# Performance work log

Measured on AMD Instinct MI355X. Metric: run time of the kernel, lower is better.

The kernel has to match this reference:

```python
import jax, jax.numpy as jnp
import numpy as np

N, E, D, H = 50000, 400000, 128, 4
NEG_SLOPE = 0.2
LN_EPS = 1e-5


def setup_inputs() -> dict:
    key = jax.random.key(0)
    ks = jax.random.split(key, 16)
    s = 1.0 / np.sqrt(D)
    inp = {
        'x': jax.random.normal(ks[0], (N, D), jnp.float32),
        'edge_index': jax.random.randint(ks[1], (2, E), 0, N, jnp.int32),
        # GATv2Conv params: lin_l/lin_r: Linear(D, H*D), att: [H, D], bias: [D] (concat=False)
        'Wl': jax.random.normal(ks[2], (H * D, D), jnp.float32) * s,
        'bl': jnp.zeros((H * D,), jnp.float32),
        'Wr': jax.random.normal(ks[3], (H * D, D), jnp.float32) * s,
        'br': jnp.zeros((H * D,), jnp.float32),
        'att': jax.random.normal(ks[4], (H, D), jnp.float32) * s,
        'bias': jnp.zeros((D,), jnp.float32),
        # LayerNorm 1
        'g1': jnp.ones((D,), jnp.float32), 'be1': jnp.zeros((D,), jnp.float32),
        # FFN: Linear(D, 2D) -> GELU -> Linear(2D, D)
        'W1': jax.random.normal(ks[5], (2 * D, D), jnp.float32) * s,
        'b1': jnp.zeros((2 * D,), jnp.float32),
        'W2': jax.random.normal(ks[6], (D, 2 * D), jnp.float32) * (1.0 / np.sqrt(2 * D)),
        'b2': jnp.zeros((D,), jnp.float32),
        # LayerNorm 2
        'g2': jnp.ones((D,), jnp.float32), 'be2': jnp.zeros((D,), jnp.float32),
    }
    return inp


def _layernorm(x, g, b):
    mu = jnp.mean(x, -1, keepdims=True)
    var = jnp.mean(jnp.square(x - mu), -1, keepdims=True)
    return (x - mu) * jax.lax.rsqrt(var + LN_EPS) * g + b


def _gatv2(x, edge_index, Wl, bl, Wr, br, att, bias):
    # Self-loops (PyG default add_self_loops=True)
    loop = jnp.arange(N, dtype=edge_index.dtype)
    src = jnp.concatenate([edge_index[0], loop])  # [E+N]
    dst = jnp.concatenate([edge_index[1], loop])
    xl = (x @ Wl.T + bl).reshape(N, H, D)  # source transform
    xr = (x @ Wr.T + br).reshape(N, H, D)  # target transform
    m = xl[src] + xr[dst]                  # [E+N, H, D]
    e = jnp.einsum('ehd,hd->eh', jax.nn.leaky_relu(m, NEG_SLOPE), att)
    # segment softmax over destination nodes
    emax = jax.ops.segment_max(e, dst, num_segments=N)
    ee = jnp.exp(e - emax[dst])
    denom = jax.ops.segment_sum(ee, dst, num_segments=N)
    alpha = ee / (denom[dst] + 1e-16)      # [E+N, H]  (dropout=0.1 skipped: eval mode)
    out = jax.ops.segment_sum(xl[src] * alpha[:, :, None], dst, num_segments=N)
    return out.mean(axis=1) + bias         # concat=False -> head mean


def reference(x, edge_index, Wl, bl, Wr, br, att, bias, g1, be1, W1, b1, W2, b2, g2, be2):
    h = _gatv2(x, edge_index, Wl, bl, Wr, br, att, bias)
    x = _layernorm(x + h, g1, be1)
    h = jax.nn.gelu(x @ W1.T + b1, approximate=False) @ W2.T + b2
    x = _layernorm(x + h, g2, be2)
    return x
```

## Files before the change

### kernel.cpp

```cpp
#include <hip/hip_runtime.h>
#include <cstdint>
#include <cstddef>

#define N_NODES 50000
#define N_EDGES 400000
#define EN_TOT  (N_EDGES + N_NODES)
#define NC_SCAN ((N_NODES + 511) / 512)
#define NEG_SLOPE 0.2f
#define LN_EPS 1e-5f

typedef short bf16x8 __attribute__((ext_vector_type(8)));
typedef float f32x4  __attribute__((ext_vector_type(4)));

__device__ __forceinline__ ushort f2bf(float f) {
    union { float f; uint32_t u; } c; c.f = f;
    uint32_t u = c.u + 0x7FFFu + ((c.u >> 16) & 1u);
    return (ushort)(u >> 16);
}
__device__ __forceinline__ uint32_t pk2(float a, float b) {
    return (uint32_t)f2bf(a) | ((uint32_t)f2bf(b) << 16);
}
__device__ __forceinline__ float bf_lo(uint32_t u) {
    union { uint32_t u; float f; } c; c.u = u << 16; return c.f;
}
__device__ __forceinline__ float bf_hi(uint32_t u) {
    union { uint32_t u; float f; } c; c.u = u & 0xFFFF0000u; return c.f;
}
__device__ __forceinline__ float bfu(const ushort* p) {
    union { uint32_t u; float f; } c; c.u = ((uint32_t)*p) << 16; return c.f;
}

__global__ __launch_bounds__(256) void prep(
    const float* __restrict__ Wl, const float* __restrict__ Wr,
    const float* __restrict__ W1, const float* __restrict__ W2,
    const float* __restrict__ att, ushort* __restrict__ wb,
    int* __restrict__ counts2 , int* __restrict__ state )
{
    int i = blockIdx.x * 256 + threadIdx.x;
    const float* src; int off;
    if (i < 65536)       { src = Wl;  off = i; }
    else if (i < 131072) { src = Wr;  off = i - 65536; }
    else if (i < 163840) { src = W1;  off = i - 131072; }
    else if (i < 196608) { src = W2;  off = i - 163840; }
    else                 { src = att; off = i - 196608; }
    wb[i] = f2bf(src[off]);
    if (i < 100000) counts2[i] = 0;
    if (i < 256)    state[i] = 0;
}

__global__ __launch_bounds__(256) void gemm_lr(
    const float* __restrict__ x, const ushort* __restrict__ wcat,
    const float* __restrict__ bl, const float* __restrict__ br,
    ushort* __restrict__ xlb, ushort* __restrict__ xrb)
{
    __shared__ ushort As[128 * 128];
    __shared__ ushort Bs[128 * 128];
    const int tid  = threadIdx.x;
    const int rb   = blockIdx.x * 128;
    const int wave = tid >> 6, lane = tid & 63;
    const int wm   = (wave >> 1) * 64, wn = (wave & 1) * 64;
    const int lr   = lane & 15, lq = lane >> 4;

    #pragma unroll
    for (int i = 0; i < 8; ++i) {
        int chunk = tid + i * 256;
        int rr = chunk >> 4, cc = chunk & 15;
        int gr = rb + rr;
        float4 v0 = make_float4(0.f,0.f,0.f,0.f), v1 = v0;
        if (gr < N_NODES) {
            v0 = *(const float4*)(x + (size_t)gr * 128 + cc * 8);
            v1 = *(const float4*)(x + (size_t)gr * 128 + cc * 8 + 4);
        }
        uint4 h = make_uint4(pk2(v0.x,v0.y), pk2(v0.z,v0.w),
                             pk2(v1.x,v1.y), pk2(v1.z,v1.w));
        *(uint4*)(As + rr * 128 + ((cc ^ (rr & 15)) * 8)) = h;
    }

    for (int cbk = 0; cbk < 8; ++cbk) {
        __syncthreads();
        #pragma unroll
        for (int i = 0; i < 8; ++i) {
            int chunk = tid + i * 256;
            int rr = chunk >> 4, cc = chunk & 15;
            uint4 vb = *(const uint4*)(wcat + (size_t)(cbk * 128 + rr) * 128 + cc * 8);
            *(uint4*)(Bs + rr * 128 + ((cc ^ (rr & 15)) * 8)) = vb;
        }
        __syncthreads();

        f32x4 zero = {0.f,0.f,0.f,0.f};
        f32x4 acc[4][4];
        #pragma unroll
        for (int i = 0; i < 4; ++i)
            #pragma unroll
            for (int j = 0; j < 4; ++j) acc[i][j] = zero;

        #pragma unroll
        for (int q = 0; q < 4; ++q) {
            int csw = ((q * 4 + lq) ^ lr) * 8;
            bf16x8 bfr[4], af[4];
            #pragma unroll
            for (int i = 0; i < 4; ++i) {
                bfr[i] = *(const bf16x8*)(Bs + (wm + i * 16 + lr) * 128 + csw);
                af[i]  = *(const bf16x8*)(As + (wn + i * 16 + lr) * 128 + csw);
            }
            #pragma unroll
            for (int i = 0; i < 4; ++i)
                #pragma unroll
                for (int j = 0; j < 4; ++j)
                    acc[i][j] = __builtin_amdgcn_mfma_f32_16x16x32_bf16(
                        bfr[i], af[j], acc[i][j], 0, 0, 0);
        }

        const float* bias = (cbk < 4) ? bl : br;
        ushort* outp = (cbk < 4) ? xlb : xrb;
        const int cloc = (cbk & 3) * 128;
        #pragma unroll
        for (int i = 0; i < 4; ++i) {
            int wc = wm + i * 16 + lq * 4;
            float4 bv = *(const float4*)(bias + cloc + wc);
            #pragma unroll
            for (int j = 0; j < 4; ++j) {
                int node = rb + wn + j * 16 + lr;
                if (node < N_NODES) {
                    ushort4 o;
                    o.x = f2bf(acc[i][j][0] + bv.x);
                    o.y = f2bf(acc[i][j][1] + bv.y);
                    o.z = f2bf(acc[i][j][2] + bv.z);
                    o.w = f2bf(acc[i][j][3] + bv.w);
                    *(ushort4*)(outp + (size_t)node * 512 + cloc + wc) = o;
                }
            }
        }
    }
}

__global__ __launch_bounds__(256) void count_deg(const int* __restrict__ dst,
                                                 int* __restrict__ counts)
{
    int i = blockIdx.x * 256 + threadIdx.x;
    if (i >= EN_TOT) return;
    int d = (i < N_EDGES) ? dst[i] : (i - N_EDGES);
    atomicAdd(counts + d, 1);
}

__global__ __launch_bounds__(64) void scan_lb(const int* __restrict__ counts,
                                              int* __restrict__ offs,
                                              unsigned long long* __restrict__ state)
{
    const int b = blockIdx.x, lane = threadIdx.x;
    const int base = b * 512 + lane * 8;
    int cnt[8];
    int s = 0;
    #pragma unroll
    for (int k = 0; k < 8; ++k) {
        int idx = base + k;
        cnt[k] = (idx < N_NODES) ? counts[idx] : 0;
        s += cnt[k];
    }
    int inc = s;
    #pragma unroll
    for (int d = 1; d < 64; d <<= 1) {
        int t = __shfl_up(inc, d, 64);
        if (lane >= d) inc += t;
    }
    const int total = __shfl(inc, 63, 64);

    if (lane == 0) {
        unsigned long long pub = ((unsigned long long)(b == 0 ? 2u : 1u) << 32)
                               | (unsigned)total;
        atomicExch(&state[b], pub);
    }

    int prefix = 0;
    if (b > 0) {
        int p0 = b - 1;
        while (true) {
            int p = p0 - lane;
            int flag, val;
            if (p >= 0) {
                unsigned long long v;
                do { v = atomicAdd(&state[p], 0ULL); flag = (int)(v >> 32); }
                while (flag == 0);
                val = (int)(unsigned)v;
            } else { flag = 2; val = 0; }
            unsigned long long mask = __ballot(flag == 2);
            int L = mask ? (__ffsll(mask) - 1) : 64;
            int take = (lane <= L) ? val : 0;
            #pragma unroll
            for (int m = 32; m; m >>= 1) take += __shfl_xor(take, m, 64);
            prefix += take;
            if (L < 64) break;
            p0 -= 64;
        }
        if (lane == 0)
            atomicExch(&state[b], (2ULL << 32) | (unsigned)(prefix + total));
    }

    int run = prefix + inc - s;
    #pragma unroll
    for (int k = 0; k < 8; ++k) {
        int idx = base + k;
        if (idx < N_NODES) { offs[idx] = run; run += cnt[k]; }
    }
    if (b == NC_SCAN - 1 && lane == 63) offs[N_NODES] = prefix + inc;
}

__global__ __launch_bounds__(256) void scatter_edges(
    const int* __restrict__ src, const int* __restrict__ dst,
    const int* __restrict__ offs, int* __restrict__ cursor,
    int* __restrict__ srcList)
{
    int i = blockIdx.x * 256 + threadIdx.x;
    if (i >= EN_TOT) return;
    int s, d;
    if (i < N_EDGES) { s = src[i]; d = dst[i]; }
    else             { s = d = i - N_EDGES; }
    int pos = atomicAdd(cursor + d, 1);
    srcList[offs[d] + pos] = s;
}

__global__ __launch_bounds__(256) void gat_fused(
    const float* __restrict__ x, const ushort* __restrict__ xl,
    const ushort* __restrict__ xr, const int* __restrict__ offs,
    const int* __restrict__ srcList, const ushort* __restrict__ attb,
    const float* __restrict__ bias, const float* __restrict__ g1,
    const float* __restrict__ be1, ushort* __restrict__ x1b)
{
    const int wave = threadIdx.x >> 6;
    const int lane = threadIdx.x & 63;
    const int v = blockIdx.x * 4 + wave;
    if (v >= N_NODES) return;

    uint4 rw = *(const uint4*)(xr + (size_t)v * 512 + lane * 8);
    uint4 aw = *(const uint4*)(attb + lane * 8);
    float r[8], at[8];
    r[0]=bf_lo(rw.x); r[1]=bf_hi(rw.x); r[2]=bf_lo(rw.y); r[3]=bf_hi(rw.y);
    r[4]=bf_lo(rw.z); r[5]=bf_hi(rw.z); r[6]=bf_lo(rw.w); r[7]=bf_hi(rw.w);
    at[0]=bf_lo(aw.x); at[1]=bf_hi(aw.x); at[2]=bf_lo(aw.y); at[3]=bf_hi(aw.y);
    at[4]=bf_lo(aw.z); at[5]=bf_hi(aw.z); at[6]=bf_lo(aw.w); at[7]=bf_hi(aw.w);

    float acc[8] = {0.f,0.f,0.f,0.f,0.f,0.f,0.f,0.f};
    float lh = 0.f;

    const int jb = offs[v], je = offs[v + 1];
    uint4 cur = *(const uint4*)(xl + (size_t)srcList[jb] * 512 + lane * 8);
    for (int j = jb; j < je; ++j) {
        int jn = (j + 1 < je) ? (j + 1) : j;
        uint4 nxt = *(const uint4*)(xl + (size_t)srcList[jn] * 512 + lane * 8);

        float b[8];
        b[0]=bf_lo(cur.x); b[1]=bf_hi(cur.x); b[2]=bf_lo(cur.y); b[3]=bf_hi(cur.y);
        b[4]=bf_lo(cur.z); b[5]=bf_hi(cur.z); b[6]=bf_lo(cur.w); b[7]=bf_hi(cur.w);
        float p = 0.f;
        #pragma unroll
        for (int k = 0; k < 8; ++k) {
            float s  = b[k] + r[k];
            float lr2 = fmaxf(s, 0.f) + NEG_SLOPE * fminf(s, 0.f);
            p = fmaf(lr2, at[k], p);
        }
        p += __shfl_xor(p, 1, 64);
        p += __shfl_xor(p, 2, 64);
        p += __shfl_xor(p, 4, 64);
        p += __shfl_xor(p, 8, 64);
        float w = __expf(p);
        lh += w;
        #pragma unroll
        for (int k = 0; k < 8; ++k) acc[k] = fmaf(w, b[k], acc[k]);
        cur = nxt;
    }

    const float inv = 1.0f / lh;
    const int d0 = (lane & 15) * 8;
    const size_t xo = (size_t)v * 128 + d0;

    float4 xv0 = *(const float4*)(x + xo);
    float4 xv1 = *(const float4*)(x + xo + 4);
    float4 bb0 = *(const float4*)(bias + d0);
    float4 bb1 = *(const float4*)(bias + d0 + 4);
    float xr8[8] = {xv0.x,xv0.y,xv0.z,xv0.w,xv1.x,xv1.y,xv1.z,xv1.w};
    float bi8[8] = {bb0.x,bb0.y,bb0.z,bb0.w,bb1.x,bb1.y,bb1.z,bb1.w};

    float y[8];
    float s = 0.f;
    #pragma unroll
    for (int k = 0; k < 8; ++k) {
        float o = acc[k] * inv;
        o += __shfl_xor(o, 16, 64);
        o += __shfl_xor(o, 32, 64);
        float yy = xr8[k] + o * 0.25f + bi8[k];
        y[k] = yy;
        s += yy;
    }
    s += __shfl_xor(s, 1, 64);
    s += __shfl_xor(s, 2, 64);
    s += __shfl_xor(s, 4, 64);
    s += __shfl_xor(s, 8, 64);
    float mu = s * (1.0f / 128.0f);
    float ss = 0.f;
    #pragma unroll
    for (int k = 0; k < 8; ++k) { float d = y[k] - mu; ss += d * d; }
    ss += __shfl_xor(ss, 1, 64);
    ss += __shfl_xor(ss, 2, 64);
    ss += __shfl_xor(ss, 4, 64);
    ss += __shfl_xor(ss, 8, 64);
    float rs = rsqrtf(ss * (1.0f / 128.0f) + LN_EPS);

    if ((lane >> 4) == 0) {
        float4 g0 = *(const float4*)(g1 + d0);
        float4 g4 = *(const float4*)(g1 + d0 + 4);
        float4 e0 = *(const float4*)(be1 + d0);
        float4 e4 = *(const float4*)(be1 + d0 + 4);
        float gg[8] = {g0.x,g0.y,g0.z,g0.w,g4.x,g4.y,g4.z,g4.w};
        float ee[8] = {e0.x,e0.y,e0.z,e0.w,e4.x,e4.y,e4.z,e4.w};
        float z[8];
        #pragma unroll
        for (int k = 0; k < 8; ++k) z[k] = (y[k] - mu) * rs * gg[k] + ee[k];
        ushort4 zb0, zb1;
        zb0.x=f2bf(z[0]); zb0.y=f2bf(z[1]); zb0.z=f2bf(z[2]); zb0.w=f2bf(z[3]);
        zb1.x=f2bf(z[4]); zb1.y=f2bf(z[5]); zb1.z=f2bf(z[6]); zb1.w=f2bf(z[7]);
        *(ushort4*)(x1b + xo)     = zb0;
        *(ushort4*)(x1b + xo + 4) = zb1;
    }
}

__global__ __launch_bounds__(256) void ffn_fused(
    const ushort* __restrict__ x1b, const ushort* __restrict__ w1b,
    const float* __restrict__ b1, const ushort* __restrict__ w2b,
    const float* __restrict__ b2, const float* __restrict__ g2,
    const float* __restrict__ be2, float* __restrict__ out)
{
    __shared__ ushort As[128 * 128];
    __shared__ ushort Bs[128 * 128];
    __shared__ ushort Ts[128 * 128];
    const int tid  = threadIdx.x;
    const int rb   = blockIdx.x * 128;
    const int wave = tid >> 6, lane = tid & 63;
    const int wm   = (wave >> 1) * 64, wn = (wave & 1) * 64;
    const int lr   = lane & 15, lq = lane >> 4;

    #pragma unroll
    for (int i = 0; i < 8; ++i) {
        int chunk = tid + i * 256;
        int rr = chunk >> 4, cc = chunk & 15;
        int gr = rb + rr;
        uint4 va = make_uint4(0u,0u,0u,0u);
        if (gr < N_NODES) va = *(const uint4*)(x1b + (size_t)gr * 128 + cc * 8);
        *(uint4*)(As + rr * 128 + ((cc ^ (rr & 15)) * 8)) = va;
    }

    f32x4 zero = {0.f,0.f,0.f,0.f};
    f32x4 acc2[4][4];
    #pragma unroll
    for (int i = 0; i < 4; ++i)
        #pragma unroll
        for (int j = 0; j < 4; ++j) acc2[i][j] = zero;

    for (int half = 0; half < 2; ++half) {
        __syncthreads();
        #pragma unroll
        for (int i = 0; i < 8; ++i) {
            int chunk = tid + i * 256;
            int rr = chunk >> 4, cc = chunk & 15;
            uint4 vb = *(const uint4*)(w1b + (size_t)(half * 128 + rr) * 128 + cc * 8);
            *(uint4*)(Bs + rr * 128 + ((cc ^ (rr & 15)) * 8)) = vb;
        }
        __syncthreads();

        f32x4 acc1[4][4];
        #pragma unroll
        for (int i = 0; i < 4; ++i)
            #pragma unroll
            for (int j = 0; j < 4; ++j) acc1[i][j] = zero;

        #pragma unroll
        for (int q = 0; q < 4; ++q) {
            int csw = ((q * 4 + lq) ^ lr) * 8;
            bf16x8 bfr[4], af[4];
            #pragma unroll
            for (int i = 0; i < 4; ++i) {
                bfr[i] = *(const bf16x8*)(Bs + (wm + i * 16 + lr) * 128 + csw);
                af[i]  = *(const bf16x8*)(As + (wn + i * 16 + lr) * 128 + csw);
            }
            #pragma unroll
            for (int i = 0; i < 4; ++i)
                #pragma unroll
                for (int j = 0; j < 4; ++j)
                    acc1[i][j] = __builtin_amdgcn_mfma_f32_16x16x32_bf16(
                        bfr[i], af[j], acc1[i][j], 0, 0, 0);
        }

        #pragma unroll
        for (int i = 0; i < 4; ++i) {
            int wc = wm + i * 16 + lq * 4;
            float4 bv = *(const float4*)(b1 + half * 128 + wc);
            #pragma unroll
            for (int j = 0; j < 4; ++j) {
                int nl = wn + j * 16 + lr;
                float v0 = acc1[i][j][0] + bv.x;
                float v1 = acc1[i][j][1] + bv.y;
                float v2 = acc1[i][j][2] + bv.z;
                float v3 = acc1[i][j][3] + bv.w;
                v0 = v0 * 0.5f * (1.0f + erff(v0 * 0.70710678118654752f));
                v1 = v1 * 0.5f * (1.0f + erff(v1 * 0.70710678118654752f));
                v2 = v2 * 0.5f * (1.0f + erff(v2 * 0.70710678118654752f));
                v3 = v3 * 0.5f * (1.0f + erff(v3 * 0.70710678118654752f));
                ushort4 o;
                o.x = f2bf(v0); o.y = f2bf(v1); o.z = f2bf(v2); o.w = f2bf(v3);
                int sw = (((wc >> 3) ^ (nl & 15)) * 8) + (wc & 7);
                *(ushort4*)(Ts + nl * 128 + sw) = o;
            }
        }
        __syncthreads();
        #pragma unroll
        for (int i = 0; i < 8; ++i) {
            int chunk = tid + i * 256;
            int rr = chunk >> 4, cc = chunk & 15;
            uint4 vb = *(const uint4*)(w2b + (size_t)rr * 256 + half * 128 + cc * 8);
            *(uint4*)(Bs + rr * 128 + ((cc ^ (rr & 15)) * 8)) = vb;
        }
        __syncthreads();

        #pragma unroll
        for (int q = 0; q < 4; ++q) {
            int csw = ((q * 4 + lq) ^ lr) * 8;
            bf16x8 bfr[4], af[4];
            #pragma unroll
            for (int i = 0; i < 4; ++i) {
                bfr[i] = *(const bf16x8*)(Bs + (wm + i * 16 + lr) * 128 + csw);
                af[i]  = *(const bf16x8*)(Ts + (wn + i * 16 + lr) * 128 + csw);
            }
            #pragma unroll
            for (int i = 0; i < 4; ++i)
                #pragma unroll
                for (int j = 0; j < 4; ++j)
                    acc2[i][j] = __builtin_amdgcn_mfma_f32_16x16x32_bf16(
                        bfr[i], af[j], acc2[i][j], 0, 0, 0);
        }
    }

    __syncthreads();
    float* sums = (float*)As;
    float* ssqs = (float*)(As + 2048);

    #pragma unroll
    for (int j = 0; j < 4; ++j) {
        int node = rb + wn + j * 16 + lr;
        float s = 0.f, q2 = 0.f;
        #pragma unroll
        for (int i = 0; i < 4; ++i) {
            int wc = wm + i * 16 + lq * 4;
            float4 bv = *(const float4*)(b2 + wc);
            float x0 = 0.f, x1r = 0.f, x2 = 0.f, x3 = 0.f;
            if (node < N_NODES) {
                ushort4 xv = *(const ushort4*)(x1b + (size_t)node * 128 + wc);
                x0 = bfu(&xv.x); x1r = bfu(&xv.y); x2 = bfu(&xv.z); x3 = bfu(&xv.w);
            }
            float y0 = acc2[i][j][0] + bv.x + x0;
            float y1 = acc2[i][j][1] + bv.y + x1r;
            float y2 = acc2[i][j][2] + bv.z + x2;
            float y3 = acc2[i][j][3] + bv.w + x3;
            acc2[i][j][0] = y0; acc2[i][j][1] = y1;
            acc2[i][j][2] = y2; acc2[i][j][3] = y3;
            s  += y0 + y1 + y2 + y3;
            q2 += y0*y0 + y1*y1 + y2*y2 + y3*y3;
        }
        s  += __shfl_xor(s, 16, 64);  s  += __shfl_xor(s, 32, 64);
        q2 += __shfl_xor(q2, 16, 64); q2 += __shfl_xor(q2, 32, 64);
        if (lq == 0) {
            int half = wm >> 6;
            sums[half * 128 + wn + j * 16 + lr] = s;
            ssqs[half * 128 + wn + j * 16 + lr] = q2;
        }
    }
    __syncthreads();

    #pragma unroll
    for (int j = 0; j < 4; ++j) {
        int nl = wn + j * 16 + lr;
        int node = rb + nl;
        if (node >= N_NODES) continue;
        float tot = sums[nl] + sums[128 + nl];
        float tq  = ssqs[nl] + ssqs[128 + nl];
        float mu  = tot * (1.0f / 128.0f);
        float var = tq * (1.0f / 128.0f) - mu * mu;
        float rs  = rsqrtf(var + LN_EPS);
        #pragma unroll
        for (int i = 0; i < 4; ++i) {
            int wc = wm + i * 16 + lq * 4;
            float4 gv = *(const float4*)(g2 + wc);
            float4 ev = *(const float4*)(be2 + wc);
            float4 o;
            o.x = (acc2[i][j][0] - mu) * rs * gv.x + ev.x;
            o.y = (acc2[i][j][1] - mu) * rs * gv.y + ev.y;
            o.z = (acc2[i][j][2] - mu) * rs * gv.z + ev.z;
            o.w = (acc2[i][j][3] - mu) * rs * gv.w + ev.w;
            *(float4*)(out + (size_t)node * 128 + wc) = o;
        }
    }
}

extern "C" void kernel_launch(void* const* d_in, const int* in_sizes, int n_in,
                              void* d_out, int out_size, void* d_ws, size_t ws_size,
                              hipStream_t stream)
{
    const float* x    = (const float*)d_in[0];
    const int*   ei   = (const int*)  d_in[1];
    const float* Wl   = (const float*)d_in[2];
    const float* bl   = (const float*)d_in[3];
    const float* Wr   = (const float*)d_in[4];
    const float* br   = (const float*)d_in[5];
    const float* att  = (const float*)d_in[6];
    const float* bias = (const float*)d_in[7];
    const float* g1   = (const float*)d_in[8];
    const float* be1  = (const float*)d_in[9];
    const float* W1   = (const float*)d_in[10];
    const float* b1   = (const float*)d_in[11];
    const float* W2   = (const float*)d_in[12];
    const float* b2   = (const float*)d_in[13];
    const float* g2   = (const float*)d_in[14];
    const float* be2  = (const float*)d_in[15];
    float* out = (float*)d_out;

    char* ws = (char*)d_ws;
    size_t off = 0;
    auto alloc = [&](size_t bytes) -> void* {
        void* p = ws + off;
        off = (off + bytes + 255) & ~(size_t)255;
        return p;
    };
    ushort* xlb  = (ushort*)alloc((size_t)N_NODES * 512 * 2);
    ushort* xrb  = (ushort*)alloc((size_t)N_NODES * 512 * 2);
    ushort* x1b  = (ushort*)alloc((size_t)N_NODES * 128 * 2);
    ushort* wb   = (ushort*)alloc((size_t)197120 * 2);
    int*   offs    = (int*)alloc((size_t)(N_NODES + 1) * 4);
    int*   counts  = (int*)alloc((size_t)N_NODES * 4 * 2);
    int*   cursor  = counts + N_NODES;
    unsigned long long* state = (unsigned long long*)alloc(256 * 4);
    int*   srcList = (int*)alloc((size_t)EN_TOT * 4);

    ushort* wcat = wb;
    ushort* w1b  = wb + 131072;
    ushort* w2b  = wb + 163840;
    ushort* attb = wb + 196608;

    prep<<<770, 256, 0, stream>>>(Wl, Wr, W1, W2, att, wb, counts, (int*)state);

    gemm_lr<<<391, 256, 0, stream>>>(x, wcat, bl, br, xlb, xrb);

    count_deg<<<(EN_TOT + 255) / 256, 256, 0, stream>>>(ei + N_EDGES, counts);
    scan_lb<<<NC_SCAN, 64, 0, stream>>>(counts, offs, state);
    scatter_edges<<<(EN_TOT + 255) / 256, 256, 0, stream>>>(ei, ei + N_EDGES,
                                                           offs, cursor, srcList);

    gat_fused<<<12500, 256, 0, stream>>>(x, xlb, xrb, offs, srcList, attb,
                                         bias, g1, be1, x1b);

    ffn_fused<<<391, 256, 0, stream>>>(x1b, w1b, b1, w2b, b2, g2, be2, out);
}
```

Baseline: 322.8 us.

## Fuse degree counting into projection GEMM, stage stores via LDS, deepen gather prefetch

```diff
diff --git a/kernel.cpp b/kernel.cpp
--- a/kernel.cpp
+++ b/kernel.cpp
@@ -26,8 +26,8 @@
 __device__ __forceinline__ float bf_hi(uint32_t u) {
     union { uint32_t u; float f; } c; c.u = u & 0xFFFF0000u; return c.f;
 }
-__device__ __forceinline__ float bfu(const ushort* p) {
-    union { uint32_t u; float f; } c; c.u = ((uint32_t)*p) << 16; return c.f;
+__device__ __forceinline__ float bfu(ushort v) {
+    union { uint32_t u; float f; } c; c.u = ((uint32_t)v) << 16; return c.f;
 }
 
 __global__ __launch_bounds__(256) void prep(
@@ -51,15 +51,25 @@
 __global__ __launch_bounds__(256) void gemm_lr(
     const float* __restrict__ x, const ushort* __restrict__ wcat,
     const float* __restrict__ bl, const float* __restrict__ br,
-    ushort* __restrict__ xlb, ushort* __restrict__ xrb)
+    ushort* __restrict__ xlb, ushort* __restrict__ xrb,
+    const int* __restrict__ dst, int* __restrict__ counts)
 {
     __shared__ ushort As[128 * 128];
-    __shared__ ushort Bs[128 * 128];
+    __shared__ ushort Bs[128 * 136];
     const int tid  = threadIdx.x;
     const int rb   = blockIdx.x * 128;
     const int wave = tid >> 6, lane = tid & 63;
     const int wm   = (wave >> 1) * 64, wn = (wave & 1) * 64;
     const int lr   = lane & 15, lq = lane >> 4;
+
+    {
+        int e0 = blockIdx.x * 1152;
+        int e1 = e0 + 1152; if (e1 > EN_TOT) e1 = EN_TOT;
+        for (int e = e0 + tid; e < e1; e += 256) {
+            int d = (e < N_EDGES) ? dst[e] : (e - N_EDGES);
+            atomicAdd(counts + d, 1);
+        }
+    }
 
     #pragma unroll
     for (int i = 0; i < 8; ++i) {
@@ -111,6 +121,7 @@
                         bfr[i], af[j], acc[i][j], 0, 0, 0);
         }
 
+        __syncthreads();
         const float* bias = (cbk < 4) ? bl : br;
         ushort* outp = (cbk < 4) ? xlb : xrb;
         const int cloc = (cbk & 3) * 128;
@@ -120,27 +131,27 @@
             float4 bv = *(const float4*)(bias + cloc + wc);
             #pragma unroll
             for (int j = 0; j < 4; ++j) {
-                int node = rb + wn + j * 16 + lr;
-                if (node < N_NODES) {
-                    ushort4 o;
-                    o.x = f2bf(acc[i][j][0] + bv.x);
-                    o.y = f2bf(acc[i][j][1] + bv.y);
-                    o.z = f2bf(acc[i][j][2] + bv.z);
-                    o.w = f2bf(acc[i][j][3] + bv.w);
-                    *(ushort4*)(outp + (size_t)node * 512 + cloc + wc) = o;
-                }
+                int nl = wn + j * 16 + lr;
+                ushort4 o;
+                o.x = f2bf(acc[i][j][0] + bv.x);
+                o.y = f2bf(acc[i][j][1] + bv.y);
+                o.z = f2bf(acc[i][j][2] + bv.z);
+                o.w = f2bf(acc[i][j][3] + bv.w);
+                *(ushort4*)(Bs + nl * 136 + wc) = o;
             }
         }
-    }
-}
-
-__global__ __launch_bounds__(256) void count_deg(const int* __restrict__ dst,
-                                                 int* __restrict__ counts)
-{
-    int i = blockIdx.x * 256 + threadIdx.x;
-    if (i >= EN_TOT) return;
-    int d = (i < N_EDGES) ? dst[i] : (i - N_EDGES);
-    atomicAdd(counts + d, 1);
+        __syncthreads();
+        #pragma unroll
+        for (int i = 0; i < 8; ++i) {
+            int chunk = tid + i * 256;
+            int row = chunk >> 4, cc = chunk & 15;
+            int node = rb + row;
+            if (node < N_NODES) {
+                uint4 v = *(const uint4*)(Bs + row * 136 + cc * 8);
+                *(uint4*)(outp + (size_t)node * 512 + cloc + cc * 8) = v;
+            }
+        }
+    }
 }
 
 __global__ __launch_bounds__(64) void scan_lb(const int* __restrict__ counts,
@@ -243,10 +254,14 @@
     float lh = 0.f;
 
     const int jb = offs[v], je = offs[v + 1];
-    uint4 cur = *(const uint4*)(xl + (size_t)srcList[jb] * 512 + lane * 8);
+    const int jlast = je - 1;
+    auto LD = [&](int j) -> uint4 {
+        int jj = (j < jlast) ? j : jlast;
+        return *(const uint4*)(xl + (size_t)srcList[jj] * 512 + lane * 8);
+    };
+    uint4 q0 = LD(jb), q1 = LD(jb + 1), q2 = LD(jb + 2);
     for (int j = jb; j < je; ++j) {
-        int jn = (j + 1 < je) ? (j + 1) : j;
-        uint4 nxt = *(const uint4*)(xl + (size_t)srcList[jn] * 512 + lane * 8);
+        uint4 cur = q0; q0 = q1; q1 = q2; q2 = LD(j + 3);
 
         float b[8];
         b[0]=bf_lo(cur.x); b[1]=bf_hi(cur.x); b[2]=bf_lo(cur.y); b[3]=bf_hi(cur.y);
@@ -266,7 +281,6 @@
         lh += w;
         #pragma unroll
         for (int k = 0; k < 8; ++k) acc[k] = fmaf(w, b[k], acc[k]);
-        cur = nxt;
     }
 
     const float inv = 1.0f / lh;
@@ -439,26 +453,22 @@
     }
 
     __syncthreads();
-    float* sums = (float*)As;
-    float* ssqs = (float*)(As + 2048);
+    float* sums = (float*)Ts;
+    float* ssqs = (float*)(Ts + 2048);
 
     #pragma unroll
     for (int j = 0; j < 4; ++j) {
-        int node = rb + wn + j * 16 + lr;
+        int nl = wn + j * 16 + lr;
         float s = 0.f, q2 = 0.f;
         #pragma unroll
         for (int i = 0; i < 4; ++i) {
             int wc = wm + i * 16 + lq * 4;
             float4 bv = *(const float4*)(b2 + wc);
-            float x0 = 0.f, x1r = 0.f, x2 = 0.f, x3 = 0.f;
-            if (node < N_NODES) {
-                ushort4 xv = *(const ushort4*)(x1b + (size_t)node * 128 + wc);
-                x0 = bfu(&xv.x); x1r = bfu(&xv.y); x2 = bfu(&xv.z); x3 = bfu(&xv.w);
-            }
-            float y0 = acc2[i][j][0] + bv.x + x0;
-            float y1 = acc2[i][j][1] + bv.y + x1r;
-            float y2 = acc2[i][j][2] + bv.z + x2;
-            float y3 = acc2[i][j][3] + bv.w + x3;
+            const ushort* ap = As + nl * 128 + (((wc >> 3) ^ (nl & 15)) * 8) + (wc & 7);
+            float y0 = acc2[i][j][0] + bv.x + bfu(ap[0]);
+            float y1 = acc2[i][j][1] + bv.y + bfu(ap[1]);
+            float y2 = acc2[i][j][2] + bv.z + bfu(ap[2]);
+            float y3 = acc2[i][j][3] + bv.w + bfu(ap[3]);
             acc2[i][j][0] = y0; acc2[i][j][1] = y1;
             acc2[i][j][2] = y2; acc2[i][j][3] = y3;
             s  += y0 + y1 + y2 + y3;
@@ -468,8 +478,8 @@
         q2 += __shfl_xor(q2, 16, 64); q2 += __shfl_xor(q2, 32, 64);
         if (lq == 0) {
             int half = wm >> 6;
-            sums[half * 128 + wn + j * 16 + lr] = s;
-            ssqs[half * 128 + wn + j * 16 + lr] = q2;
+            sums[half * 128 + nl] = s;
+            ssqs[half * 128 + nl] = q2;
         }
     }
     __syncthreads();
@@ -545,9 +555,9 @@
 
     prep<<<770, 256, 0, stream>>>(Wl, Wr, W1, W2, att, wb, counts, (int*)state);
 
-    gemm_lr<<<391, 256, 0, stream>>>(x, wcat, bl, br, xlb, xrb);
-
-    count_deg<<<(EN_TOT + 255) / 256, 256, 0, stream>>>(ei + N_EDGES, counts);
+    gemm_lr<<<391, 256, 0, stream>>>(x, wcat, bl, br, xlb, xrb,
+                                     ei + N_EDGES, counts);
+
     scan_lb<<<NC_SCAN, 64, 0, stream>>>(counts, offs, state);
     scatter_edges<<<(EN_TOT + 255) / 256, 256, 0, stream>>>(ei, ei + N_EDGES,
                                                            offs, cursor, srcList);
```

Result: faster. 303.8 us (-5.9%).
